# Optimization experiments

Measured on AMD Instinct MI355X. Metric: run time of the kernel, lower is better.

## Reference

```python
import jax, jax.numpy as jnp
import numpy as np

N = 50000   # nodes
R = 50      # relations
B = 30      # bases
F_IN = 64   # input features
H = 64      # hidden channels
C = 8       # classes
E = 1000000 # edges


def setup_inputs() -> dict:
    key = jax.random.key(0)
    ks = jax.random.split(key, 16)
    x = jax.random.normal(ks[0], (N, F_IN), jnp.float32)
    edge_index = jax.random.randint(ks[1], (2, E), 0, N)
    edge_type = jax.random.randint(ks[2], (E,), 0, R)
    inp = {"x": x, "edge_index": edge_index, "edge_type": edge_type}
    dims = [(F_IN, H), (H, H), (H, C)]
    i = 3
    for l, (din, dout) in enumerate(dims):
        s = 1.0 / np.sqrt(din)
        inp[f"bases{l}"] = jax.random.normal(ks[i], (B, din, dout), jnp.float32) * s; i += 1
        inp[f"comp{l}"] = jax.random.normal(ks[i], (R, B), jnp.float32) / np.sqrt(B); i += 1
        inp[f"root{l}"] = jax.random.normal(ks[i], (din, dout), jnp.float32) * s; i += 1
        inp[f"bias{l}"] = jnp.zeros((dout,), jnp.float32); i += 1
    return inp


def _rgcn(x, bases, comp, root, bias, src, seg):
    # Per-relation mean aggregation (PyG RGCNConv default aggr='mean'):
    # segment id = dst * R + relation. Mean of source features per (dst, rel),
    # then basis-decomposed transform (linearity lets transform follow the mean).
    din = x.shape[1]
    sums = jax.ops.segment_sum(x[src], seg, num_segments=N * R)          # [N*R, din]
    cnt = jax.ops.segment_sum(jnp.ones((seg.shape[0],), x.dtype), seg, num_segments=N * R)
    inv = jnp.where(cnt > 0, 1.0 / jnp.maximum(cnt, 1.0), 0.0)
    agg = (sums * inv[:, None]).reshape(N, R, din)                        # [N, R, din]
    t = jnp.einsum('nri,rb->nbi', agg, comp)                              # [N, B, din]
    msg = jnp.einsum('nbi,bio->no', t, bases)                             # [N, dout]
    return msg + x @ root + bias


def reference(x, edge_index, edge_type,
              bases0, comp0, root0, bias0,
              bases1, comp1, root1, bias1,
              bases2, comp2, root2, bias2):
    src, dst = edge_index[0], edge_index[1]
    seg = dst * R + edge_type
    params = [(bases0, comp0, root0, bias0),
              (bases1, comp1, root1, bias1),
              (bases2, comp2, root2, bias2)]
    x1 = x
    for b, c, r, bi in params:
        x1 = _rgcn(x, b, c, r, bi, src, seg)
        x = jax.nn.relu(x1)
    # original returns log_softmax of the last conv's pre-ReLU output
    return jax.nn.log_softmax(x1, axis=1)
```

## Files before the change

kernel.cpp:

```cpp
#include <hip/hip_runtime.h>
#include <hip/hip_bf16.h>
#include <hip/hip_fp16.h>
#include <stdint.h>

#define NN   50000
#define RR   50
#define BB   30
#define DIN  64
#define EE   1000000
#define KTOT (BB*DIN + DIN)
#define NBW  16
#define ROWE (KTOT + 8)
#define CPAD 32
#define EPAD (EE + 4*NN + 16)

typedef __attribute__((ext_vector_type(8))) short short8;
typedef __attribute__((ext_vector_type(4))) float floatx4;

#define RFL(x) __builtin_amdgcn_readfirstlane(x)


__global__ void k_hist(const int* __restrict__ dst, const int* __restrict__ et,
                       int* __restrict__ cnt) {
    int e = blockIdx.x * 256 + threadIdx.x;
    if (e < EE) {
        int d = dst[e], r = et[e];
        atomicAdd(&cnt[d * RR + r], 1);
    }
}

__global__ void k_scan1(const int* __restrict__ cnt, int* __restrict__ dcount,
                        int* __restrict__ doff, int* __restrict__ bsum) {
    __shared__ int sh[256];
    int t = threadIdx.x;
    int i = blockIdx.x * 256 + t;
    int vp = 0;
    if (i < NN) {
        const int* c = cnt + (size_t)i * RR;
        int v = 0;
#pragma unroll
        for (int r = 0; r < RR; ++r) v += c[r];
        vp = (v + 3) & ~3;
        dcount[i] = vp;
    }
    sh[t] = vp;
    __syncthreads();
    for (int s = 1; s < 256; s <<= 1) {
        int add = (t >= s) ? sh[t - s] : 0;
        __syncthreads();
        sh[t] += add;
        __syncthreads();
    }
    int incl = sh[t];
    if (i < NN) doff[i] = incl - vp;
    if (t == 255) bsum[blockIdx.x] = incl;
}

__global__ void k_scan2(int* __restrict__ bsum, int nbv) {
    __shared__ int sh[256];
    int t = threadIdx.x;
    int v = (t < nbv) ? bsum[t] : 0;
    sh[t] = v;
    __syncthreads();
    for (int s = 1; s < 256; s <<= 1) {
        int add = (t >= s) ? sh[t - s] : 0;
        __syncthreads();
        sh[t] += add;
        __syncthreads();
    }
    if (t < nbv) bsum[t] = sh[t] - v;
}

__global__ void k_scan3(int* __restrict__ doff, const int* __restrict__ bsum) {
    int i = blockIdx.x * 256 + threadIdx.x;
    if (i < NN) doff[i] += bsum[blockIdx.x];
}

__global__ void k_scatter(const int* __restrict__ src, const int* __restrict__ dst,
                          const int* __restrict__ et, const int* __restrict__ cnt,
                          const int* __restrict__ doff, int* __restrict__ cursor,
                          int2* __restrict__ ep2) {
    int e = blockIdx.x * 256 + threadIdx.x;
    if (e < EE) {
        int d = dst[e], r = et[e], s = src[e];
        int p = doff[d] + atomicAdd(&cursor[d], 1);
        float a = 1.0f / (float)cnt[d * RR + r];
        ep2[p] = make_int2(s | (r << 16), __float_as_int(a));
    }
}


__global__ void k_deghist(const int* __restrict__ dcount, int* __restrict__ dbin) {
    __shared__ int lh[256];
    int t = threadIdx.x;
    int i = blockIdx.x * 256 + t;
    lh[t] = 0;
    __syncthreads();
    if (i < NN) {
        int d = dcount[i]; d = (d > 255) ? 255 : d;
        atomicAdd(&lh[255 - d], 1);
    }
    __syncthreads();
    if (lh[t]) atomicAdd(&dbin[t], lh[t]);
}

__global__ void k_degscan(int* __restrict__ dbin) {
    __shared__ int sh[256];
    int t = threadIdx.x;
    int v = dbin[t];
    sh[t] = v;
    __syncthreads();
    for (int s = 1; s < 256; s <<= 1) {
        int add = (t >= s) ? sh[t - s] : 0;
        __syncthreads();
        sh[t] += add;
        __syncthreads();
    }
    dbin[t] = sh[t] - v;
}

__global__ void k_degscatter(const int* __restrict__ dcount, const int* __restrict__ dbin,
                             int* __restrict__ dcur, int* __restrict__ order) {
    __shared__ int lh[256], lbase[256];
    int t = threadIdx.x;
    int i = blockIdx.x * 256 + t;
    lh[t] = 0;
    __syncthreads();
    int b = 0, lpos = 0;
    if (i < NN) {
        int d = dcount[i]; d = (d > 255) ? 255 : d;
        b = 255 - d;
        lpos = atomicAdd(&lh[b], 1);
    }
    __syncthreads();
    lbase[t] = lh[t] ? atomicAdd(&dcur[t], lh[t]) : 0;
    __syncthreads();
    if (i < NN) order[dbin[b] + lbase[b] + lpos] = i;
}

__global__ void k_cast_x(const float* __restrict__ x, __hip_bfloat16* __restrict__ h) {
    int i = blockIdx.x * 256 + threadIdx.x;
    if (i < NN * DIN) h[i] = __float2bfloat16(x[i]);
}

__global__ void k_prep_comp3(const float* __restrict__ c0, const float* __restrict__ c1,
                             const float* __restrict__ c2, __half* __restrict__ cp) {
    int idx = blockIdx.x * 256 + threadIdx.x;
    if (idx < 3 * RR * CPAD) {
        int l = idx / (RR * CPAD);
        int rem = idx - l * (RR * CPAD);
        int r = rem / CPAD, i = rem - r * CPAD;
        const float* c = (l == 0) ? c0 : (l == 1) ? c1 : c2;
        cp[idx] = (i < BB) ? __float2half(c[r * BB + i]) : __float2half(0.f);
    }
}

__global__ void k_prep_w3(const float* __restrict__ b0, const float* __restrict__ r0,
                          const float* __restrict__ b1, const float* __restrict__ r1,
                          const float* __restrict__ b2, const float* __restrict__ r2,
                          short* __restrict__ wt) {
    int idx = blockIdx.x * 256 + threadIdx.x;
    if (idx >= 144 * KTOT) return;
    int row = idx / KTOT, k = idx - row * KTOT;
    const float* bs; const float* rt; int o, dout;
    if (row < 64)       { bs = b0; rt = r0; o = row;        dout = 64; }
    else if (row < 128) { bs = b1; rt = r1; o = row - 64;   dout = 64; }
    else                { bs = b2; rt = r2; o = row - 128;  dout = 8;  }
    float v = 0.f;
    if (o < dout)
        v = (k < BB * DIN) ? bs[k * dout + o] : rt[(k - BB * DIN) * dout + o];
    __hip_bfloat16 hb = __float2bfloat16(v);
    wt[idx] = *reinterpret_cast<const short*>(&hb);
}


struct RecS { int x0, a0i, x1, a1i, x2, a2i, x3, a3i; };

#define LOADREC4(u, VA, VB) do {                                                \
    const int _u = ((u) < nch) ? (u) : (nch - 1);                               \
    const int4* _p = ep4 + (base4V + 2 * _u);                                   \
    VA = _p[0]; VB = _p[1];                                                     \
} while (0)

#define RFLREC(VA, VB, S) do {                                                  \
    S.x0 = RFL((VA).x); S.a0i = RFL((VA).y);                                    \
    S.x1 = RFL((VA).z); S.a1i = RFL((VA).w);                                    \
    S.x2 = RFL((VB).x); S.a2i = RFL((VB).y);                                    \
    S.x3 = RFL((VB).z); S.a3i = RFL((VB).w);                                    \
} while (0)

#define GATH1(sx) ((unsigned)xin16[((sx) & 0xFFFF) * DIN + lane])

#define EDGE_FMA_PRE(M0, M1, M2, M3, _ai, _g) do {                              \
    const float _xvf = __uint_as_float((unsigned)(_g) << 16) * __int_as_float(_ai); \
    const __half _xh = __float2half(_xvf);                                      \
    const __half2 _xv2 = __halves2half2(_xh, _xh);                              \
    const __half2* _p0 = reinterpret_cast<const __half2*>(&(M0));               \
    const __half2* _p1 = reinterpret_cast<const __half2*>(&(M1));               \
    const __half2* _p2 = reinterpret_cast<const __half2*>(&(M2));               \
    const __half2* _p3 = reinterpret_cast<const __half2*>(&(M3));               \
    acc[0]  = __hfma2(_p0[0], _xv2, acc[0]);                                    \
    acc[1]  = __hfma2(_p0[1], _xv2, acc[1]);                                    \
    acc[2]  = __hfma2(_p0[2], _xv2, acc[2]);                                    \
    acc[3]  = __hfma2(_p0[3], _xv2, acc[3]);                                    \
    acc[4]  = __hfma2(_p1[0], _xv2, acc[4]);                                    \
    acc[5]  = __hfma2(_p1[1], _xv2, acc[5]);                                    \
    acc[6]  = __hfma2(_p1[2], _xv2, acc[6]);                                    \
    acc[7]  = __hfma2(_p1[3], _xv2, acc[7]);                                    \
    acc[8]  = __hfma2(_p2[0], _xv2, acc[8]);                                    \
    acc[9]  = __hfma2(_p2[1], _xv2, acc[9]);                                    \
    acc[10] = __hfma2(_p2[2], _xv2, acc[10]);                                   \
    acc[11] = __hfma2(_p2[3], _xv2, acc[11]);                                   \
    acc[12] = __hfma2(_p3[0], _xv2, acc[12]);                                   \
    acc[13] = __hfma2(_p3[1], _xv2, acc[13]);                                   \
    acc[14] = __hfma2(_p3[2], _xv2, acc[14]);                                   \
    acc[15] = __hfma2(_p3[3], _xv2, acc[15]);                                   \
} while (0)

#define ITER(tt, VA, VB) do {                                                   \
    RecS s3; RFLREC(VA, VB, s3);                                                \
    const int4* _cp0 = (const int4*)(compH + ((unsigned)s0.x0 >> 16) * CPAD);   \
    const int4* _cp1 = (const int4*)(compH + ((unsigned)s0.x1 >> 16) * CPAD);   \
    const int4* _cp2 = (const int4*)(compH + ((unsigned)s0.x2 >> 16) * CPAD);   \
    const int4* _cp3 = (const int4*)(compH + ((unsigned)s0.x3 >> 16) * CPAD);   \
    int4 _e0a = _cp0[0], _e0b = _cp0[1], _e0c = _cp0[2], _e0d = _cp0[3];        \
    int4 _e1a = _cp1[0], _e1b = _cp1[1], _e1c = _cp1[2], _e1d = _cp1[3];        \
    int4 _e2a = _cp2[0], _e2b = _cp2[1], _e2c = _cp2[2], _e2d = _cp2[3];        \
    int4 _e3a = _cp3[0], _e3b = _cp3[1], _e3c = _cp3[2], _e3d = _cp3[3];        \
    unsigned w0 = GATH1(s3.x0), w1 = GATH1(s3.x1);                              \
    unsigned w2 = GATH1(s3.x2), w3 = GATH1(s3.x3);                              \
    LOADREC4((tt) + 5, VA, VB);                                                 \
    EDGE_FMA_PRE(_e0a, _e0b, _e0c, _e0d, s0.a0i, g0);                           \
    EDGE_FMA_PRE(_e1a, _e1b, _e1c, _e1d, s0.a1i, g1);                           \
    EDGE_FMA_PRE(_e2a, _e2b, _e2c, _e2d, s0.a2i, g2);                           \
    EDGE_FMA_PRE(_e3a, _e3b, _e3c, _e3d, s0.a3i, g3);                           \
    s0 = s1; s1 = s2; s2 = s3;                                                  \
    g0 = h0; g1 = h1; g2 = h2; g3 = h3;                                         \
    h0 = i0; h1 = i1; h2 = i2; h3 = i3;                                         \
    i0 = w0; i1 = w1; i2 = w2; i3 = w3;                                         \
} while (0)

template <int DOUT, bool RELU>
__global__ __launch_bounds__(1024, 8)
void k_fused(const __hip_bfloat16* __restrict__ xin,
             const int2* __restrict__ ep2,
             const int* __restrict__ doff, const int* __restrict__ dcount,
             const int* __restrict__ order,
             const __half* __restrict__ compH,
             const short* __restrict__ Wt,
             const float* __restrict__ bias,
             void* __restrict__ outp) {
    __shared__ __align__(16) char smem_raw[NBW * ROWE * 2];
    auto t_tile = reinterpret_cast<__hip_bfloat16(*)[ROWE]>(smem_raw);
    const unsigned short* xin16 = reinterpret_cast<const unsigned short*>(xin);
    const int tid  = threadIdx.x;
    const int lane = tid & 63;
    const int wv   = RFL(tid >> 6);
    const int node0 = blockIdx.x * NBW;

    {
        const int j = wv;
        const int n = RFL(order[node0 + j]);
        __half2 acc[16];
#pragma unroll
        for (int u = 0; u < 16; ++u)
            acc[u] = __halves2half2(__float2half(0.f), __float2half(0.f));
        const int beg = RFL(doff[n]);
        const int nch = RFL(dcount[n]) >> 2;
        const unsigned selfb = (unsigned)xin16[n * DIN + lane];

        if (nch > 0) {
            const int4* ep4 = reinterpret_cast<const int4*>(ep2);
            const int base4V = __builtin_amdgcn_ds_bpermute(0, beg >> 1);
            int4 vaA, vbA, vaB, vbB;
            RecS s0, s1, s2;
            LOADREC4(0, vaA, vbA);
            LOADREC4(1, vaB, vbB);
            RFLREC(vaA, vbA, s0);
            unsigned g0 = GATH1(s0.x0), g1 = GATH1(s0.x1);
            unsigned g2 = GATH1(s0.x2), g3 = GATH1(s0.x3);
            LOADREC4(2, vaA, vbA);
            RFLREC(vaB, vbB, s1);
            unsigned h0 = GATH1(s1.x0), h1 = GATH1(s1.x1);
            unsigned h2 = GATH1(s1.x2), h3 = GATH1(s1.x3);
            LOADREC4(3, vaB, vbB);
            RFLREC(vaA, vbA, s2);
            unsigned i0 = GATH1(s2.x0), i1 = GATH1(s2.x1);
            unsigned i2 = GATH1(s2.x2), i3 = GATH1(s2.x3);
            LOADREC4(4, vaA, vbA);
            int t = 0;
            for (; t + 2 <= nch; t += 2) {
                ITER(t,     vaB, vbB);
                ITER(t + 1, vaA, vbA);
            }
            if (t < nch) ITER(t, vaB, vbB);
        }
#pragma unroll
        for (int b = 0; b < BB; ++b) {
            const float v = (b & 1) ? __high2float(acc[b >> 1]) : __low2float(acc[b >> 1]);
            t_tile[j][b * DIN + lane] = __float2bfloat16(v);
        }
        t_tile[j][BB * DIN + lane] =
            __float2bfloat16(__uint_as_float(selfb << 16));
    }
    __syncthreads();

    const int m = lane & 15;
    const int q = lane >> 4;
    int kk0, nsteps, col_base, kpart;
    if (DOUT == 64) {
        kpart = wv >> 2;
        col_base = (wv & 3) * 16;
        kk0    = (kpart <= 1) ? kpart * 16 : (kpart == 2 ? 32 : 47);
        nsteps = (kpart <= 1) ? 16 : 15;
    } else {
        kpart = wv;
        col_base = 0;
        kk0    = (kpart < 14) ? kpart * 4 : (kpart == 14 ? 56 : 59);
        nsteps = (kpart < 14) ? 4 : 3;
    }
    const __hip_bfloat16* arow = &t_tile[m][q * 8];
    const short* brow = Wt + (size_t)(col_base + m) * KTOT + q * 8;

    floatx4 acc0 = {0.f, 0.f, 0.f, 0.f};
    floatx4 acc1 = {0.f, 0.f, 0.f, 0.f};
    int s = 0;
    for (; s + 2 <= nsteps; s += 2) {
        const int kk = kk0 + s;
        short8 a0 = *reinterpret_cast<const short8*>(arow + kk * 32);
        short8 b0 = *reinterpret_cast<const short8*>(brow + kk * 32);
        short8 a1 = *reinterpret_cast<const short8*>(arow + (kk + 1) * 32);
        short8 b1 = *reinterpret_cast<const short8*>(brow + (kk + 1) * 32);
        acc0 = __builtin_amdgcn_mfma_f32_16x16x32_bf16(a0, b0, acc0, 0, 0, 0);
        acc1 = __builtin_amdgcn_mfma_f32_16x16x32_bf16(a1, b1, acc1, 0, 0, 0);
    }
    if (s < nsteps) {
        const int kk = kk0 + s;
        short8 a0 = *reinterpret_cast<const short8*>(arow + kk * 32);
        short8 b0 = *reinterpret_cast<const short8*>(brow + kk * 32);
        acc0 = __builtin_amdgcn_mfma_f32_16x16x32_bf16(a0, b0, acc0, 0, 0, 0);
    }
    floatx4 P = acc0 + acc1;

    __syncthreads();
    float* red = (float*)smem_raw;

    if (DOUT == 64) {
        if (kpart > 0) {
            const int slot = (wv & 3) * 3 + (kpart - 1);
            const int off = (slot * 64 + lane) * 6;
            red[off] = P[0]; red[off + 1] = P[1]; red[off + 2] = P[2]; red[off + 3] = P[3];
        }
        __syncthreads();
        if (kpart == 0) {
#pragma unroll
            for (int t = 0; t < 3; ++t) {
                const int off = (((wv & 3) * 3 + t) * 64 + lane) * 6;
                P[0] += red[off]; P[1] += red[off + 1];
                P[2] += red[off + 2]; P[3] += red[off + 3];
            }
            const int o = col_base + m;
            const float bi = bias[o];
#pragma unroll
            for (int r = 0; r < 4; ++r) {
                const int n = order[node0 + q * 4 + r];
                float v = P[r] + bi;
                if (RELU) {
                    v = fmaxf(v, 0.f);
                    reinterpret_cast<__hip_bfloat16*>(outp)[(size_t)n * DOUT + o] =
                        __float2bfloat16(v);
                } else {
                    reinterpret_cast<float*>(outp)[(size_t)n * DOUT + o] = v;
                }
            }
        }
    } else {
        if (kpart > 0) {
            const int off = ((kpart - 1) * 64 + lane) * 6;
            red[off] = P[0]; red[off + 1] = P[1]; red[off + 2] = P[2]; red[off + 3] = P[3];
        }
        __syncthreads();
        if (kpart == 0) {
#pragma unroll
            for (int w = 0; w < 15; ++w) {
                const int off = (w * 64 + lane) * 6;
                P[0] += red[off]; P[1] += red[off + 1];
                P[2] += red[off + 2]; P[3] += red[off + 3];
            }
            if (m < DOUT) {
                const int o = m;
                const float bi = bias[o];
#pragma unroll
                for (int r = 0; r < 4; ++r) {
                    const int n = order[node0 + q * 4 + r];
                    reinterpret_cast<float*>(outp)[(size_t)n * DOUT + o] = P[r] + bi;
                }
            }
        }
    }
}

__global__ void k_lsm(const float* __restrict__ pre, float* __restrict__ out) {
    int n = blockIdx.x * 256 + threadIdx.x;
    if (n < NN) {
        float v[8];
        float mx = -1e30f;
#pragma unroll
        for (int c = 0; c < 8; ++c) { v[c] = pre[n * 8 + c]; mx = fmaxf(mx, v[c]); }
        float s = 0.f;
#pragma unroll
        for (int c = 0; c < 8; ++c) s += expf(v[c] - mx);
        float ls = logf(s);
#pragma unroll
        for (int c = 0; c < 8; ++c) out[n * 8 + c] = v[c] - mx - ls;
    }
}

extern "C" void kernel_launch(void* const* d_in, const int* in_sizes, int n_in,
                              void* d_out, int out_size, void* d_ws, size_t ws_size,
                              hipStream_t stream) {
    const float* x     = (const float*)d_in[0];
    const int*   eidx  = (const int*)d_in[1];
    const int*   etype = (const int*)d_in[2];
    const float* bases0 = (const float*)d_in[3];
    const float* comp0  = (const float*)d_in[4];
    const float* root0  = (const float*)d_in[5];
    const float* bias0  = (const float*)d_in[6];
    const float* bases1 = (const float*)d_in[7];
    const float* comp1  = (const float*)d_in[8];
    const float* root1  = (const float*)d_in[9];
    const float* bias1  = (const float*)d_in[10];
    const float* bases2 = (const float*)d_in[11];
    const float* comp2  = (const float*)d_in[12];
    const float* root2  = (const float*)d_in[13];
    const float* bias2  = (const float*)d_in[14];
    const int* srcp = eidx;
    const int* dstp = eidx + EE;

    char* p = (char*)d_ws;
    auto carve = [&](size_t bytes) -> char* {
        char* r = p;
        p += (bytes + 255) & ~(size_t)255;
        return r;
    };
    int*  cnt    = (int*)carve((size_t)NN * RR * sizeof(int));
    int*  dcount = (int*)carve((size_t)NN * sizeof(int));
    int*  cursor = (int*)carve((size_t)NN * sizeof(int));
    int*  doff   = (int*)carve((size_t)NN * sizeof(int));
    int*  bsum   = (int*)carve(256 * sizeof(int));
    int*  dbin   = (int*)carve(256 * sizeof(int));
    int*  dcur   = (int*)carve(256 * sizeof(int));
    int*  order  = (int*)carve((size_t)NN * sizeof(int));
    int2* ep2    = (int2*)carve((size_t)EPAD * sizeof(int2));
    __hip_bfloat16* h0 = (__hip_bfloat16*)carve((size_t)NN * DIN * 2);
    __hip_bfloat16* h1 = (__hip_bfloat16*)carve((size_t)NN * DIN * 2);
    __hip_bfloat16* h2 = (__hip_bfloat16*)carve((size_t)NN * DIN * 2);
    float* pre = (float*)carve((size_t)NN * 8 * sizeof(float));
    short* wtA = (short*)carve((size_t)144 * KTOT * sizeof(short));
    __half* cpA = (__half*)carve((size_t)3 * RR * CPAD * sizeof(__half));

    hipMemsetAsync(cnt, 0, (size_t)NN * (RR + 2) * sizeof(int) + 512, stream);
    hipMemsetAsync(dbin, 0, 2048, stream);
    hipMemsetAsync(ep2, 0, (size_t)EPAD * sizeof(int2), stream);

    const int EB = (EE + 255) / 256;
    const int NB = (NN + 255) / 256;
    k_hist<<<EB, 256, 0, stream>>>(dstp, etype, cnt);
    k_scan1<<<NB, 256, 0, stream>>>(cnt, dcount, doff, bsum);
    k_scan2<<<1, 256, 0, stream>>>(bsum, NB);
    k_scan3<<<NB, 256, 0, stream>>>(doff, bsum);
    k_scatter<<<EB, 256, 0, stream>>>(srcp, dstp, etype, cnt, doff, cursor, ep2);
    k_deghist<<<NB, 256, 0, stream>>>(dcount, dbin);
    k_degscan<<<1, 256, 0, stream>>>(dbin);
    k_degscatter<<<NB, 256, 0, stream>>>(dcount, dbin, dcur, order);
    k_cast_x<<<(NN * DIN + 255) / 256, 256, 0, stream>>>(x, h0);
    k_prep_comp3<<<(3 * RR * CPAD + 255) / 256, 256, 0, stream>>>(comp0, comp1, comp2, cpA);
    k_prep_w3<<<(144 * KTOT + 255) / 256, 256, 0, stream>>>(bases0, root0, bases1, root1,
                                                            bases2, root2, wtA);

    short* wt0 = wtA;
    short* wt1 = wtA + (size_t)64 * KTOT;
    short* wt2 = wtA + (size_t)128 * KTOT;
    __half* cp0 = cpA;
    __half* cp1 = cpA + RR * CPAD;
    __half* cp2 = cpA + 2 * RR * CPAD;

    const int NF = NN / NBW;
    k_fused<64, true ><<<NF, 1024, 0, stream>>>(h0, ep2, doff, dcount, order, cp0, wt0, bias0, (void*)h1);
    k_fused<64, true ><<<NF, 1024, 0, stream>>>(h1, ep2, doff, dcount, order, cp1, wt1, bias1, (void*)h2);
    k_fused<8,  false><<<NF, 1024, 0, stream>>>(h2, ep2, doff, dcount, order, cp2, wt2, bias2, (void*)pre);
    k_lsm<<<NB, 256, 0, stream>>>(pre, (float*)d_out);
}
```

Baseline: 555.5 us.

## Pad edge lists to multiples of eight and restructure the gather pipeline

Per-node edge counts are now padded to a multiple of eight instead of four, and the fused aggregation loop handles eight edge records per iteration. It uses a simpler two-stage prefetch (records two steps ahead, gathers one step ahead) with a scheduling barrier, replacing the deeper four-record rotating pipeline. The x-to-bf16 cast is also vectorized to four elements per thread. The larger padding adds more zero-weight dummy edges per node, and the shallower prefetch may hide less gather latency in exchange for fewer live registers.

After: 557.0 us. Within noise of the previous version (+0.3%).

```diff
diff --git a/kernel.cpp b/kernel.cpp
--- a/kernel.cpp
+++ b/kernel.cpp
@@ -12,7 +12,7 @@
 #define NBW  16
 #define ROWE (KTOT + 8)
 #define CPAD 32
-#define EPAD (EE + 4*NN + 16)
+#define EPAD (EE + 8*NN + 32)
 
 typedef __attribute__((ext_vector_type(8))) short short8;
 typedef __attribute__((ext_vector_type(4))) float floatx4;
@@ -40,7 +40,7 @@
         int v = 0;
 #pragma unroll
         for (int r = 0; r < RR; ++r) v += c[r];
-        vp = (v + 3) & ~3;
+        vp = (v + 7) & ~7;
         dcount[i] = vp;
     }
     sh[t] = vp;
@@ -140,7 +140,15 @@
 
 __global__ void k_cast_x(const float* __restrict__ x, __hip_bfloat16* __restrict__ h) {
     int i = blockIdx.x * 256 + threadIdx.x;
-    if (i < NN * DIN) h[i] = __float2bfloat16(x[i]);
+    if (i < NN * DIN / 4) {
+        float4 v = reinterpret_cast<const float4*>(x)[i];
+        ushort4 o;
+        o.x = (ushort)(__bfloat16_as_ushort(__float2bfloat16(v.x)));
+        o.y = (ushort)(__bfloat16_as_ushort(__float2bfloat16(v.y)));
+        o.z = (ushort)(__bfloat16_as_ushort(__float2bfloat16(v.z)));
+        o.w = (ushort)(__bfloat16_as_ushort(__float2bfloat16(v.w)));
+        reinterpret_cast<ushort4*>(h)[i] = o;
+    }
 }
 
 __global__ void k_prep_comp3(const float* __restrict__ c0, const float* __restrict__ c1,
@@ -174,31 +182,24 @@
 }
 
 
-struct RecS { int x0, a0i, x1, a1i, x2, a2i, x3, a3i; };
-
-#define LOADREC4(u, VA, VB) do {                                                \
-    const int _u = ((u) < nch) ? (u) : (nch - 1);                               \
-    const int4* _p = ep4 + (base4V + 2 * _u);                                   \
-    VA = _p[0]; VB = _p[1];                                                     \
+#define LOADR8(u, R0, R1, R2, R3) do {                                          \
+    const int _u = ((u) < nit) ? (u) : (nit - 1);                               \
+    R0 = rec4[4 * _u];     R1 = rec4[4 * _u + 1];                               \
+    R2 = rec4[4 * _u + 2]; R3 = rec4[4 * _u + 3];                               \
 } while (0)
 
-#define RFLREC(VA, VB, S) do {                                                  \
-    S.x0 = RFL((VA).x); S.a0i = RFL((VA).y);                                    \
-    S.x1 = RFL((VA).z); S.a1i = RFL((VA).w);                                    \
-    S.x2 = RFL((VB).x); S.a2i = RFL((VB).y);                                    \
-    S.x3 = RFL((VB).z); S.a3i = RFL((VB).w);                                    \
-} while (0)
-
 #define GATH1(sx) ((unsigned)xin16[((sx) & 0xFFFF) * DIN + lane])
 
-#define EDGE_FMA_PRE(M0, M1, M2, M3, _ai, _g) do {                              \
+#define EDGE_FMA1(_sx, _ai, _g) do {                                            \
+    const int4* _cr = (const int4*)(compH + ((unsigned)(_sx) >> 16) * CPAD);    \
+    int4 _m0 = _cr[0], _m1 = _cr[1], _m2 = _cr[2], _m3 = _cr[3];                \
     const float _xvf = __uint_as_float((unsigned)(_g) << 16) * __int_as_float(_ai); \
     const __half _xh = __float2half(_xvf);                                      \
     const __half2 _xv2 = __halves2half2(_xh, _xh);                              \
-    const __half2* _p0 = reinterpret_cast<const __half2*>(&(M0));               \
-    const __half2* _p1 = reinterpret_cast<const __half2*>(&(M1));               \
-    const __half2* _p2 = reinterpret_cast<const __half2*>(&(M2));               \
-    const __half2* _p3 = reinterpret_cast<const __half2*>(&(M3));               \
+    const __half2* _p0 = reinterpret_cast<const __half2*>(&_m0);                \
+    const __half2* _p1 = reinterpret_cast<const __half2*>(&_m1);                \
+    const __half2* _p2 = reinterpret_cast<const __half2*>(&_m2);                \
+    const __half2* _p3 = reinterpret_cast<const __half2*>(&_m3);                \
     acc[0]  = __hfma2(_p0[0], _xv2, acc[0]);                                    \
     acc[1]  = __hfma2(_p0[1], _xv2, acc[1]);                                    \
     acc[2]  = __hfma2(_p0[2], _xv2, acc[2]);                                    \
@@ -217,29 +218,6 @@
     acc[15] = __hfma2(_p3[3], _xv2, acc[15]);                                   \
 } while (0)
 
-#define ITER(tt, VA, VB) do {                                                   \
-    RecS s3; RFLREC(VA, VB, s3);                                                \
-    const int4* _cp0 = (const int4*)(compH + ((unsigned)s0.x0 >> 16) * CPAD);   \
-    const int4* _cp1 = (const int4*)(compH + ((unsigned)s0.x1 >> 16) * CPAD);   \
-    const int4* _cp2 = (const int4*)(compH + ((unsigned)s0.x2 >> 16) * CPAD);   \
-    const int4* _cp3 = (const int4*)(compH + ((unsigned)s0.x3 >> 16) * CPAD);   \
-    int4 _e0a = _cp0[0], _e0b = _cp0[1], _e0c = _cp0[2], _e0d = _cp0[3];        \
-    int4 _e1a = _cp1[0], _e1b = _cp1[1], _e1c = _cp1[2], _e1d = _cp1[3];        \
-    int4 _e2a = _cp2[0], _e2b = _cp2[1], _e2c = _cp2[2], _e2d = _cp2[3];        \
-    int4 _e3a = _cp3[0], _e3b = _cp3[1], _e3c = _cp3[2], _e3d = _cp3[3];        \
-    unsigned w0 = GATH1(s3.x0), w1 = GATH1(s3.x1);                              \
-    unsigned w2 = GATH1(s3.x2), w3 = GATH1(s3.x3);                              \
-    LOADREC4((tt) + 5, VA, VB);                                                 \
-    EDGE_FMA_PRE(_e0a, _e0b, _e0c, _e0d, s0.a0i, g0);                           \
-    EDGE_FMA_PRE(_e1a, _e1b, _e1c, _e1d, s0.a1i, g1);                           \
-    EDGE_FMA_PRE(_e2a, _e2b, _e2c, _e2d, s0.a2i, g2);                           \
-    EDGE_FMA_PRE(_e3a, _e3b, _e3c, _e3d, s0.a3i, g3);                           \
-    s0 = s1; s1 = s2; s2 = s3;                                                  \
-    g0 = h0; g1 = h1; g2 = h2; g3 = h3;                                         \
-    h0 = i0; h1 = i1; h2 = i2; h3 = i3;                                         \
-    i0 = w0; i1 = w1; i2 = w2; i3 = w3;                                         \
-} while (0)
-
 template <int DOUT, bool RELU>
 __global__ __launch_bounds__(1024, 8)
 void k_fused(const __hip_bfloat16* __restrict__ xin,
@@ -266,34 +244,39 @@
         for (int u = 0; u < 16; ++u)
             acc[u] = __halves2half2(__float2half(0.f), __float2half(0.f));
         const int beg = RFL(doff[n]);
-        const int nch = RFL(dcount[n]) >> 2;
+        const int nit = RFL(dcount[n]) >> 3;
         const unsigned selfb = (unsigned)xin16[n * DIN + lane];
 
-        if (nch > 0) {
-            const int4* ep4 = reinterpret_cast<const int4*>(ep2);
-            const int base4V = __builtin_amdgcn_ds_bpermute(0, beg >> 1);
-            int4 vaA, vbA, vaB, vbB;
-            RecS s0, s1, s2;
-            LOADREC4(0, vaA, vbA);
-            LOADREC4(1, vaB, vbB);
-            RFLREC(vaA, vbA, s0);
-            unsigned g0 = GATH1(s0.x0), g1 = GATH1(s0.x1);
-            unsigned g2 = GATH1(s0.x2), g3 = GATH1(s0.x3);
-            LOADREC4(2, vaA, vbA);
-            RFLREC(vaB, vbB, s1);
-            unsigned h0 = GATH1(s1.x0), h1 = GATH1(s1.x1);
-            unsigned h2 = GATH1(s1.x2), h3 = GATH1(s1.x3);
-            LOADREC4(3, vaB, vbB);
-            RFLREC(vaA, vbA, s2);
-            unsigned i0 = GATH1(s2.x0), i1 = GATH1(s2.x1);
-            unsigned i2 = GATH1(s2.x2), i3 = GATH1(s2.x3);
-            LOADREC4(4, vaA, vbA);
-            int t = 0;
-            for (; t + 2 <= nch; t += 2) {
-                ITER(t,     vaB, vbB);
-                ITER(t + 1, vaA, vbA);
+        if (nit > 0) {
+            const int4* rec4 = (const int4*)(ep2 + beg);
+            int4 A0, A1, A2, A3, B0, B1, B2, B3, C0, C1, C2, C3;
+            LOADR8(0, A0, A1, A2, A3);
+            LOADR8(1, B0, B1, B2, B3);
+            unsigned g0 = GATH1(RFL(A0.x)), g1 = GATH1(RFL(A0.z));
+            unsigned g2 = GATH1(RFL(A1.x)), g3 = GATH1(RFL(A1.z));
+            unsigned g4 = GATH1(RFL(A2.x)), g5 = GATH1(RFL(A2.z));
+            unsigned g6 = GATH1(RFL(A3.x)), g7 = GATH1(RFL(A3.z));
+
+            for (int t = 0; t < nit; ++t) {
+                unsigned h0 = GATH1(RFL(B0.x)), h1 = GATH1(RFL(B0.z));
+                unsigned h2 = GATH1(RFL(B1.x)), h3 = GATH1(RFL(B1.z));
+                unsigned h4 = GATH1(RFL(B2.x)), h5 = GATH1(RFL(B2.z));
+                unsigned h6 = GATH1(RFL(B3.x)), h7 = GATH1(RFL(B3.z));
+                EDGE_FMA1(RFL(A0.x), RFL(A0.y), g0);
+                EDGE_FMA1(RFL(A0.z), RFL(A0.w), g1);
+                EDGE_FMA1(RFL(A1.x), RFL(A1.y), g2);
+                EDGE_FMA1(RFL(A1.z), RFL(A1.w), g3);
+                EDGE_FMA1(RFL(A2.x), RFL(A2.y), g4);
+                EDGE_FMA1(RFL(A2.z), RFL(A2.w), g5);
+                EDGE_FMA1(RFL(A3.x), RFL(A3.y), g6);
+                EDGE_FMA1(RFL(A3.z), RFL(A3.w), g7);
+                __builtin_amdgcn_sched_barrier(0);
+                LOADR8(t + 2, C0, C1, C2, C3);
+                A0 = B0; A1 = B1; A2 = B2; A3 = B3;
+                B0 = C0; B1 = C1; B2 = C2; B3 = C3;
+                g0 = h0; g1 = h1; g2 = h2; g3 = h3;
+                g4 = h4; g5 = h5; g6 = h6; g7 = h7;
             }
-            if (t < nch) ITER(t, vaB, vbB);
         }
 #pragma unroll
         for (int b = 0; b < BB; ++b) {
@@ -473,7 +456,7 @@
     k_deghist<<<NB, 256, 0, stream>>>(dcount, dbin);
     k_degscan<<<1, 256, 0, stream>>>(dbin);
     k_degscatter<<<NB, 256, 0, stream>>>(dcount, dbin, dcur, order);
-    k_cast_x<<<(NN * DIN + 255) / 256, 256, 0, stream>>>(x, h0);
+    k_cast_x<<<(NN * DIN / 4 + 255) / 256, 256, 0, stream>>>(x, h0);
     k_prep_comp3<<<(3 * RR * CPAD + 255) / 256, 256, 0, stream>>>(comp0, comp1, comp2, cpA);
     k_prep_w3<<<(144 * KTOT + 255) / 256, 256, 0, stream>>>(bases0, root0, bases1, root1,
                                                             bases2, root2, wtA);
```
